# Performance work log

Measured on AMD Instinct MI355X. Metric: run time of the kernel, lower is better.

## Reference

```python
import jax, jax.numpy as jnp
import numpy as np

N, E, D, ED, H = 50000, 800000, 128, 16, 1
EPS = 1e-5


def setup_inputs() -> dict:
    key = jax.random.key(0)
    ks = jax.random.split(key, 12)
    return {
        "x": jax.random.normal(ks[0], (N, D), jnp.float32),
        "edge_index": jax.random.randint(ks[1], (2, E), 0, N),
        "edge_attr": jax.random.normal(ks[2], (E, ED), jnp.float32),
        # GATv2Conv params
        "W_l": jax.random.normal(ks[3], (D, H * D), jnp.float32) / np.sqrt(D),
        "b_l": jnp.zeros((H * D,), jnp.float32),
        "W_r": jax.random.normal(ks[4], (D, H * D), jnp.float32) / np.sqrt(D),
        "b_r": jnp.zeros((H * D,), jnp.float32),
        "W_e": jax.random.normal(ks[5], (ED, H * D), jnp.float32) / np.sqrt(ED),
        "att": jax.random.normal(ks[6], (H, D), jnp.float32) * 0.1,
        "bias_gat": jnp.zeros((D,), jnp.float32),
        # block params
        "weight1": jax.random.normal(ks[7], (2,), jnp.float32),
        "bn1_gamma": jnp.ones((D,), jnp.float32),
        "bn1_beta": jnp.zeros((D,), jnp.float32),
        "conv_w": jax.random.normal(ks[8], (D, D, 3), jnp.float32) / np.sqrt(3 * D),
        "conv_b": jnp.zeros((D,), jnp.float32),
        "weight2": jax.random.normal(ks[9], (2,), jnp.float32),
        "bn2_gamma": jnp.ones((D,), jnp.float32),
        "bn2_beta": jnp.zeros((D,), jnp.float32),
    }


def _batch_norm(z, gamma, beta):
    # NodeLevelBatchNorm in training mode: stats over all nodes of the batch graph
    mu = z.mean(axis=0)
    var = z.var(axis=0)
    return (z - mu) * jax.lax.rsqrt(var + EPS) * gamma + beta


def _gatv2(x, edge_index, edge_attr, W_l, b_l, W_r, b_r, W_e, att, bias_gat):
    n = x.shape[0]
    # add self loops with edge_attr fill_value=0
    loop = jnp.arange(n)
    src = jnp.concatenate([edge_index[0], loop])  # message sources j
    dst = jnp.concatenate([edge_index[1], loop])  # message targets i
    x_l = (x @ W_l + b_l).reshape(n, H, D)
    x_r = (x @ W_r + b_r).reshape(n, H, D)
    e = (edge_attr @ W_e).reshape(-1, H, D)
    e = jnp.concatenate([e, jnp.zeros((n, H, D), e.dtype)], axis=0)  # zeros: lin_edge(0)=0
    # [E+N, H, D] edge messages
    m = jax.nn.leaky_relu(x_l[src] + x_r[dst] + e, negative_slope=0.2)
    logits = jnp.einsum('ehc,hc->eh', m, att)  # [E+N, H]
    # softmax grouped by target node (every node has a self loop -> no empty segments)
    lmax = jax.ops.segment_max(logits, dst, num_segments=n)
    p = jnp.exp(logits - lmax[dst])
    denom = jax.ops.segment_sum(p, dst, num_segments=n)
    alpha = p / denom[dst]
    out = jax.ops.segment_sum(alpha[:, :, None] * x_l[src], dst, num_segments=n)  # [N,H,D]
    return out.mean(axis=1) + bias_gat  # concat=False -> head mean


def reference(x, edge_index, edge_attr, W_l, b_l, W_r, b_r, W_e, att, bias_gat,
              weight1, bn1_gamma, bn1_beta, conv_w, conv_b, weight2,
              bn2_gamma, bn2_beta):
    attn_feat = _gatv2(x, edge_index, edge_attr, W_l, b_l, W_r, b_r, W_e, att, bias_gat)
    w1 = jax.nn.softmax(weight1)
    z = w1[0] * x + w1[1] * attn_feat
    z = _batch_norm(z, bn1_gamma, bn1_beta)
    # Conv1d over the node dimension: [1, C, N] -> [1, C, N]
    z1 = jax.lax.conv_general_dilated(
        z.T[None], conv_w, window_strides=(1,), padding=[(1, 1)],
        dimension_numbers=('NCH', 'OIH', 'NCH'))
    z1 = z1[0].T + conv_b  # [N, C]
    z1 = jax.nn.leaky_relu(z1, negative_slope=0.01)  # dropout inactive in eval
    w2 = jax.nn.softmax(weight2)
    z = w2[0] * z + w2[1] * z1
    z = _batch_norm(z, bn2_gamma, bn2_beta)
    return z
```

## Files before the change

kernel.cpp:

```cpp
#include <hip/hip_runtime.h>
#include <hip/hip_bf16.h>
#include <math.h>

#define DD 128
#define EPSBN 1e-5f

typedef float f2 __attribute__((ext_vector_type(2)));

__device__ __forceinline__ float4 f4_add(float4 a, float4 b) {
    return make_float4(a.x + b.x, a.y + b.y, a.z + b.z, a.w + b.w);
}
__device__ __forceinline__ float4 f4_fma(float a, float4 b, float4 c) {
    c.x = fmaf(a, b.x, c.x); c.y = fmaf(a, b.y, c.y);
    c.z = fmaf(a, b.z, c.z); c.w = fmaf(a, b.w, c.w);
    return c;
}
__device__ __forceinline__ float leakyf(float v, float s) { return v > 0.f ? v : s * v; }

__device__ __forceinline__ unsigned short f2bf(float f) {
    unsigned u = __float_as_uint(f);
    return (unsigned short)((u + 0x7fffu + ((u >> 16) & 1u)) >> 16);
}
__device__ __forceinline__ f2 bfu2f2(unsigned u) {
    f2 r;
    r.x = __uint_as_float(u << 16);
    r.y = __uint_as_float(u & 0xFFFF0000u);
    return r;
}
__device__ __forceinline__ f2 leaky2(f2 v, float s) {
    f2 z = (f2)0.f;
    return __builtin_elementwise_max(v, z) + s * __builtin_elementwise_min(v, z);
}

__global__ __launch_bounds__(256) void k_prep(const float* __restrict__ conv_w, float* __restrict__ wT,
                                              int* __restrict__ counts, float* __restrict__ stats,
                                              int n, int nstats) {
    int idx = blockIdx.x * 256 + threadIdx.x;
    if (idx < 3 * 128 * 128) {
        int k = idx >> 14;
        int r = idx & 16383;
        int ci = r >> 7, co = r & 127;
        wT[idx] = conv_w[(size_t)co * 384 + ci * 3 + k];
    }
    int z = idx - 3 * 128 * 128;
    if (z >= 0) {
        if (z < n) counts[z] = 0;
        else if (z - n < nstats) stats[z - n] = 0.f;
    }
}

__global__ __launch_bounds__(256) void k_gemm_xlxr(
    const float* __restrict__ x, const float* __restrict__ Wl, const float* __restrict__ bl,
    const float* __restrict__ Wr, const float* __restrict__ br,
    float* __restrict__ XR, unsigned short* __restrict__ XLh, int n)
{
    __shared__ float As[64 * 33];
    __shared__ float Bs[32 * 256];
    int tid = threadIdx.x;
    int r0 = blockIdx.x * 64;
    int tx = tid & 31, ty = tid >> 5;

    float4 accL[8], accR[8];
    #pragma unroll
    for (int j = 0; j < 8; ++j) {
        accL[j] = make_float4(0.f, 0.f, 0.f, 0.f);
        accR[j] = make_float4(0.f, 0.f, 0.f, 0.f);
    }

    for (int k0 = 0; k0 < 128; k0 += 32) {
        for (int idx = tid; idx < 64 * 32; idx += 256) {
            int lrow = idx >> 5, kk = idx & 31;
            int g = r0 + lrow;
            As[lrow * 33 + kk] = (g < n) ? x[(size_t)g * DD + k0 + kk] : 0.f;
        }
        for (int idx = tid; idx < 2048; idx += 256) {
            int kk = idx >> 6, co4 = idx & 63;
            float4 v;
            if (co4 < 32) v = ((const float4*)Wl)[(size_t)(k0 + kk) * 32 + co4];
            else          v = ((const float4*)Wr)[(size_t)(k0 + kk) * 32 + (co4 - 32)];
            ((float4*)Bs)[kk * 64 + co4] = v;
        }
        __syncthreads();

        #pragma unroll 4
        for (int kk = 0; kk < 32; ++kk) {
            float a[8];
            #pragma unroll
            for (int j = 0; j < 8; ++j) a[j] = As[(ty * 8 + j) * 33 + kk];
            float4 bL = ((float4*)Bs)[kk * 64 + tx];
            float4 bR = ((float4*)Bs)[kk * 64 + 32 + tx];
            #pragma unroll
            for (int j = 0; j < 8; ++j) {
                accL[j] = f4_fma(a[j], bL, accL[j]);
                accR[j] = f4_fma(a[j], bR, accR[j]);
            }
        }
        __syncthreads();
    }

    float4 blv = ((const float4*)bl)[tx];
    float4 brv = ((const float4*)br)[tx];
    #pragma unroll
    for (int j = 0; j < 8; ++j) {
        int row = r0 + ty * 8 + j;
        if (row < n) {
            float4 L4 = f4_add(accL[j], blv);
            ((float4*)(XR + (size_t)row * DD))[tx] = f4_add(accR[j], brv);
            uint2 hp;
            hp.x = (unsigned)f2bf(L4.x) | ((unsigned)f2bf(L4.y) << 16);
            hp.y = (unsigned)f2bf(L4.z) | ((unsigned)f2bf(L4.w) << 16);
            ((uint2*)(XLh + (size_t)row * DD))[tx] = hp;
        }
    }
}

__global__ __launch_bounds__(256) void k_hist(const int* __restrict__ dst, int* __restrict__ counts, int e) {
    int idx = blockIdx.x * 256 + threadIdx.x;
    if (idx < e) atomicAdd(&counts[dst[idx]], 1);
}

__global__ __launch_bounds__(256) void k_scan1(const int* __restrict__ counts,
                                               int* __restrict__ offsets, int* __restrict__ bsum, int n) {
    __shared__ int tmp[256];
    int t = threadIdx.x;
    int i = blockIdx.x * 256 + t;
    int v = (i < n) ? counts[i] : 0;
    tmp[t] = v;
    __syncthreads();
    for (int off = 1; off < 256; off <<= 1) {
        int u = (t >= off) ? tmp[t - off] : 0;
        __syncthreads();
        tmp[t] += u;
        __syncthreads();
    }
    if (i < n) offsets[i] = tmp[t] - v;
    if (t == 255) bsum[blockIdx.x] = tmp[255];
}

__global__ __launch_bounds__(1024) void k_scan2(int* __restrict__ bsum, int nchunks) {
    __shared__ int tmp[1024];
    int t = threadIdx.x;
    int v = (t < nchunks) ? bsum[t] : 0;
    tmp[t] = v;
    __syncthreads();
    for (int off = 1; off < 1024; off <<= 1) {
        int u = (t >= off) ? tmp[t - off] : 0;
        __syncthreads();
        tmp[t] += u;
        __syncthreads();
    }
    if (t < nchunks) bsum[t] = tmp[t] - v;
    if (t == 0) bsum[nchunks] = tmp[nchunks - 1];
}

__global__ __launch_bounds__(256) void k_scan3(int* __restrict__ offsets, int* __restrict__ cursor,
                                               const int* __restrict__ bsum, int n, int nchunks) {
    int i = blockIdx.x * 256 + threadIdx.x;
    if (i < n) {
        int o = offsets[i] + bsum[i >> 8];
        offsets[i] = o;
        cursor[i] = o;
    }
    if (i == n) offsets[n] = bsum[nchunks];
}

__global__ __launch_bounds__(256) void k_scatter(const int* __restrict__ src, const int* __restrict__ dst,
                                                 int* __restrict__ cursor, int2* __restrict__ epair, int e) {
    int idx = blockIdx.x * 256 + threadIdx.x;
    if (idx >= e) return;
    int d = dst[idx];
    int pos = atomicAdd(&cursor[d], 1);
    epair[pos] = make_int2(idx, src[idx]);
}

#define GAT_LOAD(q_, U0_, U1_, A0_, A1_)                                        \
    {                                                                           \
        int2 g0_ = epair[q_], g1_ = epair[(q_) + 1];                            \
        int e0_ = __builtin_amdgcn_readfirstlane(g0_.x);                        \
        int s0_ = __builtin_amdgcn_readfirstlane(g0_.y);                        \
        int e1_ = __builtin_amdgcn_readfirstlane(g1_.x);                        \
        int s1_ = __builtin_amdgcn_readfirstlane(g1_.y);                        \
        U0_ = XLu[(size_t)s0_ * 64 + lane];                                     \
        U1_ = XLu[(size_t)s1_ * 64 + lane];                                     \
        const float* q0_ = edge_attr + (size_t)e0_ * 16;                        \
        const float* q1_ = edge_attr + (size_t)e1_ * 16;                        \
        _Pragma("unroll")                                                       \
        for (int k_ = 0; k_ < 16; ++k_) { A0_[k_] = q0_[k_]; A1_[k_] = q1_[k_]; } \
    }

#define GAT_COMPUTE(U0_, U1_, A0_, A1_)                                         \
    {                                                                           \
        f2 x0_ = bfu2f2(U0_), x1_ = bfu2f2(U1_);                                \
        f2 ev0_ = (f2)0.f, ev1_ = (f2)0.f;                                      \
        _Pragma("unroll")                                                       \
        for (int k_ = 0; k_ < 16; ++k_) {                                       \
            ev0_ = __builtin_elementwise_fma((f2)A0_[k_], w2[k_], ev0_);        \
            ev1_ = __builtin_elementwise_fma((f2)A1_[k_], w2[k_], ev1_);        \
        }                                                                       \
        f2 m0_ = leaky2(x0_ + xr2 + ev0_, 0.2f);                                \
        f2 m1_ = leaky2(x1_ + xr2 + ev1_, 0.2f);                                \
        float l0_ = m0_.x * att2.x + m0_.y * att2.y;                            \
        float l1_ = m1_.x * att2.x + m1_.y * att2.y;                            \
        _Pragma("unroll")                                                       \
        for (int off_ = 32; off_ > 0; off_ >>= 1) {                             \
            l0_ += __shfl_xor(l0_, off_, 64);                                   \
            l1_ += __shfl_xor(l1_, off_, 64);                                   \
        }                                                                       \
        float g0_ = __expf(l0_), g1_ = __expf(l1_);                             \
        S += g0_ + g1_;                                                         \
        axy = __builtin_elementwise_fma((f2)g0_, x0_, axy);                     \
        axy = __builtin_elementwise_fma((f2)g1_, x1_, axy);                     \
    }

__global__ __launch_bounds__(256) void k_gat(
    const unsigned short* __restrict__ XLh, const float* __restrict__ XR,
    const float* __restrict__ x,
    const int2* __restrict__ epair, const int* __restrict__ offsets,
    const float* __restrict__ edge_attr, const float* __restrict__ We,
    const float* __restrict__ att, const float* __restrict__ bias_gat,
    const float* __restrict__ weight1, float* __restrict__ Z, int n, int nwaves)
{
    int wid  = blockIdx.x * 4 + (threadIdx.x >> 6);
    int lane = threadIdx.x & 63;
    int c = lane * 2;
    const unsigned* __restrict__ XLu = (const unsigned*)XLh;

    f2 w2[16];
    #pragma unroll
    for (int k = 0; k < 16; ++k) w2[k] = *(const f2*)(We + k * DD + c);
    f2 att2 = *(const f2*)(att + c);
    f2 bg   = *(const f2*)(bias_gat + c);
    float w0 = weight1[0], w1v = weight1[1];
    float mw = fmaxf(w0, w1v);
    float e0w = __expf(w0 - mw), e1w = __expf(w1v - mw);
    float winv = 1.f / (e0w + e1w);
    float w1x = e0w * winv, w1a = e1w * winv;

    for (int i = wid; i < n; i += nwaves) {
        f2 xr2 = *(const f2*)(XR + (size_t)i * DD + c);
        f2 xli = bfu2f2(XLu[(size_t)i * 64 + lane]);

        f2 ms = leaky2(xli + xr2, 0.2f);
        float sl = ms.x * att2.x + ms.y * att2.y;
        #pragma unroll
        for (int off = 32; off > 0; off >>= 1) sl += __shfl_xor(sl, off, 64);
        float gs = __expf(sl);
        float S = gs;
        f2 axy = gs * xli;

        int p  = __builtin_amdgcn_readfirstlane(offsets[i]);
        int pe = __builtin_amdgcn_readfirstlane(offsets[i + 1]);
        int cnt = pe - p;
        int np = cnt >> 1;

        unsigned uA0, uA1, uB0, uB1;
        float aA0[16], aA1[16], aB0[16], aB1[16];

        if (np > 0) {
            GAT_LOAD(p, uA0, uA1, aA0, aA1);
            int t = 0;
            for (;;) {
                if (t + 1 < np) GAT_LOAD(p + 2 * (t + 1), uB0, uB1, aB0, aB1);
                GAT_COMPUTE(uA0, uA1, aA0, aA1);
                if (++t >= np) break;
                if (t + 1 < np) GAT_LOAD(p + 2 * (t + 1), uA0, uA1, aA0, aA1);
                GAT_COMPUTE(uB0, uB1, aB0, aB1);
                if (++t >= np) break;
            }
        }
        if (cnt & 1) {
            int2 ej = epair[pe - 1];
            int eid = __builtin_amdgcn_readfirstlane(ej.x);
            int srn = __builtin_amdgcn_readfirstlane(ej.y);
            unsigned u = XLu[(size_t)srn * 64 + lane];
            const float* pa = edge_attr + (size_t)eid * 16;
            f2 ev = (f2)0.f;
            #pragma unroll
            for (int k = 0; k < 16; ++k) ev = __builtin_elementwise_fma((f2)pa[k], w2[k], ev);
            f2 x0 = bfu2f2(u);
            f2 m = leaky2(x0 + xr2 + ev, 0.2f);
            float l = m.x * att2.x + m.y * att2.y;
            #pragma unroll
            for (int off = 32; off > 0; off >>= 1) l += __shfl_xor(l, off, 64);
            float g = __expf(l);
            S += g;
            axy = __builtin_elementwise_fma((f2)g, x0, axy);
        }

        float rl = 1.f / S;
        f2 av = axy * rl + bg;
        f2 xv = *(const f2*)(x + (size_t)i * DD + c);
        f2 zv = w1x * xv + w1a * av;
        *(f2*)(Z + (size_t)i * DD + c) = zv;
    }
}

__global__ __launch_bounds__(256) void k_bn_stats(const float* __restrict__ Zin,
                                                  float* __restrict__ sums, float* __restrict__ sumsq, int n) {
    __shared__ float4 Ls[8][32];
    __shared__ float4 Lq[8][32];
    int tid = threadIdx.x;
    int cg = tid & 31, ry = tid >> 5;
    float4 s = make_float4(0.f, 0.f, 0.f, 0.f), q = s;
    for (int r = blockIdx.x * 8 + ry; r < n; r += gridDim.x * 8) {
        float4 v = ((const float4*)(Zin + (size_t)r * DD))[cg];
        s = f4_add(s, v);
        q.x = fmaf(v.x, v.x, q.x); q.y = fmaf(v.y, v.y, q.y);
        q.z = fmaf(v.z, v.z, q.z); q.w = fmaf(v.w, v.w, q.w);
    }
    Ls[ry][cg] = s; Lq[ry][cg] = q;
    __syncthreads();
    if (tid < 32) {
        float4 ts = Ls[0][tid], tq = Lq[0][tid];
        #pragma unroll
        for (int j = 1; j < 8; ++j) { ts = f4_add(ts, Ls[j][tid]); tq = f4_add(tq, Lq[j][tid]); }
        atomicAdd(&sums[tid * 4 + 0], ts.x); atomicAdd(&sums[tid * 4 + 1], ts.y);
        atomicAdd(&sums[tid * 4 + 2], ts.z); atomicAdd(&sums[tid * 4 + 3], ts.w);
        atomicAdd(&sumsq[tid * 4 + 0], tq.x); atomicAdd(&sumsq[tid * 4 + 1], tq.y);
        atomicAdd(&sumsq[tid * 4 + 2], tq.z); atomicAdd(&sumsq[tid * 4 + 3], tq.w);
    }
}

__global__ __launch_bounds__(128) void k_bn_finish(const float* __restrict__ sums, const float* __restrict__ sumsq,
                                                   const float* __restrict__ gamma, const float* __restrict__ beta,
                                                   float* __restrict__ scale, float* __restrict__ shift, int n) {
    int t = threadIdx.x;
    if (t >= 128) return;
    float fn = (float)n;
    float mu = sums[t] / fn;
    float var = sumsq[t] / fn - mu * mu;
    float rstd = rsqrtf(var + EPSBN);
    float sc = gamma[t] * rstd;
    scale[t] = sc;
    shift[t] = fmaf(-mu, sc, beta[t]);
}

__global__ __launch_bounds__(256) void k_conv(
    const float* __restrict__ Z, const float* __restrict__ scale1, const float* __restrict__ shift1,
    const float* __restrict__ wT, const float* __restrict__ conv_b,
    const float* __restrict__ weight2, float* __restrict__ Z2, int n)
{
    __shared__ float As[66 * 33];
    __shared__ float Bs[3 * 32 * 128];
    int tid = threadIdx.x;
    int r0 = blockIdx.x * 64;
    int tx = tid & 31, ty = tid >> 5;
    int rbase = ty * 8;

    float4 acc[8];
    #pragma unroll
    for (int j = 0; j < 8; ++j) acc[j] = make_float4(0.f, 0.f, 0.f, 0.f);

    for (int ci0 = 0; ci0 < 128; ci0 += 32) {
        for (int idx = tid; idx < 66 * 32; idx += 256) {
            int lrow = idx >> 5, ci = idx & 31;
            int g = r0 - 1 + lrow;
            int cc = ci0 + ci;
            float v = 0.f;
            if (g >= 0 && g < n)
                v = fmaf(Z[(size_t)g * DD + cc], scale1[cc], shift1[cc]);
            As[lrow * 33 + ci] = v;
        }
        for (int idx = tid; idx < 3072; idx += 256) {
            int k = idx >> 10;
            int r = idx & 1023;
            int ci = r >> 5, co4 = r & 31;
            ((float4*)Bs)[idx] = ((const float4*)wT)[(size_t)k * 4096 + (ci0 + ci) * 32 + co4];
        }
        __syncthreads();

        #pragma unroll 2
        for (int ci = 0; ci < 32; ++ci) {
            float a[10];
            #pragma unroll
            for (int j = 0; j < 10; ++j) a[j] = As[(rbase + j) * 33 + ci];
            float4 b0 = ((float4*)Bs)[(0 * 32 + ci) * 32 + tx];
            float4 b1 = ((float4*)Bs)[(1 * 32 + ci) * 32 + tx];
            float4 b2 = ((float4*)Bs)[(2 * 32 + ci) * 32 + tx];
            #pragma unroll
            for (int j = 0; j < 8; ++j) {
                acc[j] = f4_fma(a[j],     b0, acc[j]);
                acc[j] = f4_fma(a[j + 1], b1, acc[j]);
                acc[j] = f4_fma(a[j + 2], b2, acc[j]);
            }
        }
        __syncthreads();
    }

    float w0 = weight2[0], w1v = weight2[1];
    float mw = fmaxf(w0, w1v);
    float e0 = __expf(w0 - mw), e1 = __expf(w1v - mw);
    float winv = 1.f / (e0 + e1);
    float w2x = e0 * winv, w2a = e1 * winv;

    float4 cb = ((const float4*)conv_b)[tx];
    float4 sc1 = ((const float4*)scale1)[tx];
    float4 sh1 = ((const float4*)shift1)[tx];
    #pragma unroll
    for (int j = 0; j < 8; ++j) {
        int row = r0 + rbase + j;
        if (row >= n) break;
        float4 z1 = f4_add(acc[j], cb);
        z1.x = leakyf(z1.x, 0.01f); z1.y = leakyf(z1.y, 0.01f);
        z1.z = leakyf(z1.z, 0.01f); z1.w = leakyf(z1.w, 0.01f);
        float4 zv = ((const float4*)(Z + (size_t)row * DD))[tx];
        float4 zbn;
        zbn.x = fmaf(zv.x, sc1.x, sh1.x); zbn.y = fmaf(zv.y, sc1.y, sh1.y);
        zbn.z = fmaf(zv.z, sc1.z, sh1.z); zbn.w = fmaf(zv.w, sc1.w, sh1.w);
        float4 o;
        o.x = w2x * zbn.x + w2a * z1.x; o.y = w2x * zbn.y + w2a * z1.y;
        o.z = w2x * zbn.z + w2a * z1.z; o.w = w2x * zbn.w + w2a * z1.w;
        ((float4*)(Z2 + (size_t)row * DD))[tx] = o;
    }
}

__global__ __launch_bounds__(256) void k_final(const float* __restrict__ Z2,
                                               const float* __restrict__ scale2, const float* __restrict__ shift2,
                                               float* __restrict__ out, int total4) {
    int idx = blockIdx.x * 256 + threadIdx.x;
    if (idx >= total4) return;
    int c4 = idx & 31;
    float4 v = ((const float4*)Z2)[idx];
    float4 sc = ((const float4*)scale2)[c4];
    float4 sh = ((const float4*)shift2)[c4];
    float4 r;
    r.x = fmaf(v.x, sc.x, sh.x); r.y = fmaf(v.y, sc.y, sh.y);
    r.z = fmaf(v.z, sc.z, sh.z); r.w = fmaf(v.w, sc.w, sh.w);
    ((float4*)out)[idx] = r;
}

extern "C" void kernel_launch(void* const* d_in, const int* in_sizes, int n_in,
                              void* d_out, int out_size, void* d_ws, size_t ws_size,
                              hipStream_t stream)
{
    const float* x          = (const float*)d_in[0];
    const int*   edge_index = (const int*)d_in[1];
    const float* edge_attr  = (const float*)d_in[2];
    const float* W_l        = (const float*)d_in[3];
    const float* b_l        = (const float*)d_in[4];
    const float* W_r        = (const float*)d_in[5];
    const float* b_r        = (const float*)d_in[6];
    const float* W_e        = (const float*)d_in[7];
    const float* att        = (const float*)d_in[8];
    const float* bias_gat   = (const float*)d_in[9];
    const float* weight1    = (const float*)d_in[10];
    const float* bn1_gamma  = (const float*)d_in[11];
    const float* bn1_beta   = (const float*)d_in[12];
    const float* conv_w     = (const float*)d_in[13];
    const float* conv_b     = (const float*)d_in[14];
    const float* weight2    = (const float*)d_in[15];
    const float* bn2_gamma  = (const float*)d_in[16];
    const float* bn2_beta   = (const float*)d_in[17];

    int n = in_sizes[0] / DD;
    int e = in_sizes[1] / 2;
    int nchunks = (n + 255) / 256;

    float* XR = (float*)d_ws;
    float* Z  = XR + (size_t)n * DD;
    float* wT = Z + (size_t)n * DD;
    float* stats = wT + 49152;
    float* sums1 = stats,       *sumsq1 = stats + 128;
    float* sums2 = stats + 256, *sumsq2 = stats + 384;
    float* scale1 = stats + 512, *shift1 = stats + 640;
    float* scale2 = stats + 768, *shift2 = stats + 896;
    int* counts  = (int*)(stats + 1024);
    int* offsets = counts + n;
    int* cursor  = offsets + n + 2;
    int* bsum    = cursor + n;
    int2* epair  = (int2*)(bsum + ((nchunks + 2) & ~1));
    unsigned short* XLh = (unsigned short*)(epair + e);
    float* Z2 = XR;

    const int* src = edge_index;
    const int* dst = edge_index + e;

    const int nwaves = 8192;

    k_prep<<<(3 * 128 * 128 + n + 512 + 255) / 256, 256, 0, stream>>>(conv_w, wT, counts, stats, n, 512);
    k_gemm_xlxr<<<(n + 63) / 64, 256, 0, stream>>>(x, W_l, b_l, W_r, b_r, XR, XLh, n);
    k_hist<<<(e + 255) / 256, 256, 0, stream>>>(dst, counts, e);
    k_scan1<<<nchunks, 256, 0, stream>>>(counts, offsets, bsum, n);
    k_scan2<<<1, 1024, 0, stream>>>(bsum, nchunks);
    k_scan3<<<(n + 256) / 256, 256, 0, stream>>>(offsets, cursor, bsum, n, nchunks);
    k_scatter<<<(e + 255) / 256, 256, 0, stream>>>(src, dst, cursor, epair, e);
    k_gat<<<nwaves / 4, 256, 0, stream>>>(XLh, XR, x, epair, offsets,
                                          edge_attr, W_e, att, bias_gat, weight1, Z, n, nwaves);
    k_bn_stats<<<256, 256, 0, stream>>>(Z, sums1, sumsq1, n);
    k_bn_finish<<<1, 128, 0, stream>>>(sums1, sumsq1, bn1_gamma, bn1_beta, scale1, shift1, n);
    k_conv<<<(n + 63) / 64, 256, 0, stream>>>(Z, scale1, shift1, wT, conv_b, weight2, Z2, n);
    k_bn_stats<<<256, 256, 0, stream>>>(Z2, sums2, sumsq2, n);
    k_bn_finish<<<1, 128, 0, stream>>>(sums2, sumsq2, bn2_gamma, bn2_beta, scale2, shift2, n);
    k_final<<<(n * 32 + 255) / 256, 256, 0, stream>>>(Z2, scale2, shift2, (float*)d_out, n * 32);
}
```

Before: 612.9 us.

## Batch GAT edges in fours with cooperative edge_attr loads; fuse BN2 stats into conv

The GAT aggregation loop now handles four edges per step instead of two. Each lane loads one edge_attr element, and the values are staged through a per-wave double-buffered LDS slot, replacing sixteen redundant per-lane scalar loads per edge. Separately, the conv kernel accumulates per-channel sum and sum-of-squares of its output and adds them to the global stats with atomics, which removes the separate k_bn_stats pass that re-read Z2. The costs are extra LDS traffic and a tail loop for up to three leftover edges. The global float atomics also make the summation order nondeterministic.

```diff
diff --git a/kernel.cpp b/kernel.cpp
--- a/kernel.cpp
+++ b/kernel.cpp
@@ -173,44 +173,71 @@
     epair[pos] = make_int2(idx, src[idx]);
 }
 
-#define GAT_LOAD(q_, U0_, U1_, A0_, A1_)                                        \
-    {                                                                           \
-        int2 g0_ = epair[q_], g1_ = epair[(q_) + 1];                            \
-        int e0_ = __builtin_amdgcn_readfirstlane(g0_.x);                        \
-        int s0_ = __builtin_amdgcn_readfirstlane(g0_.y);                        \
-        int e1_ = __builtin_amdgcn_readfirstlane(g1_.x);                        \
-        int s1_ = __builtin_amdgcn_readfirstlane(g1_.y);                        \
-        U0_ = XLu[(size_t)s0_ * 64 + lane];                                     \
-        U1_ = XLu[(size_t)s1_ * 64 + lane];                                     \
-        const float* q0_ = edge_attr + (size_t)e0_ * 16;                        \
-        const float* q1_ = edge_attr + (size_t)e1_ * 16;                        \
-        _Pragma("unroll")                                                       \
-        for (int k_ = 0; k_ < 16; ++k_) { A0_[k_] = q0_[k_]; A1_[k_] = q1_[k_]; } \
-    }
-
-#define GAT_COMPUTE(U0_, U1_, A0_, A1_)                                         \
-    {                                                                           \
-        f2 x0_ = bfu2f2(U0_), x1_ = bfu2f2(U1_);                                \
-        f2 ev0_ = (f2)0.f, ev1_ = (f2)0.f;                                      \
-        _Pragma("unroll")                                                       \
-        for (int k_ = 0; k_ < 16; ++k_) {                                       \
-            ev0_ = __builtin_elementwise_fma((f2)A0_[k_], w2[k_], ev0_);        \
-            ev1_ = __builtin_elementwise_fma((f2)A1_[k_], w2[k_], ev1_);        \
-        }                                                                       \
-        f2 m0_ = leaky2(x0_ + xr2 + ev0_, 0.2f);                                \
-        f2 m1_ = leaky2(x1_ + xr2 + ev1_, 0.2f);                                \
-        float l0_ = m0_.x * att2.x + m0_.y * att2.y;                            \
-        float l1_ = m1_.x * att2.x + m1_.y * att2.y;                            \
-        _Pragma("unroll")                                                       \
-        for (int off_ = 32; off_ > 0; off_ >>= 1) {                             \
-            l0_ += __shfl_xor(l0_, off_, 64);                                   \
-            l1_ += __shfl_xor(l1_, off_, 64);                                   \
-        }                                                                       \
-        float g0_ = __expf(l0_), g1_ = __expf(l1_);                             \
-        S += g0_ + g1_;                                                         \
-        axy = __builtin_elementwise_fma((f2)g0_, x0_, axy);                     \
-        axy = __builtin_elementwise_fma((f2)g1_, x1_, axy);                     \
-    }
+
+#define EPROJ(EB_, J_, EV_) {                                                   \
+    const float4* e4_ = ((const float4*)(EB_)) + (J_) * 4;                      \
+    float4 a0_ = e4_[0], a1_ = e4_[1], a2_ = e4_[2], a3_ = e4_[3];              \
+    f2 v_ = (f2)0.f;                                                            \
+    v_ = __builtin_elementwise_fma((f2)a0_.x, w2[0],  v_);                      \
+    v_ = __builtin_elementwise_fma((f2)a0_.y, w2[1],  v_);                      \
+    v_ = __builtin_elementwise_fma((f2)a0_.z, w2[2],  v_);                      \
+    v_ = __builtin_elementwise_fma((f2)a0_.w, w2[3],  v_);                      \
+    v_ = __builtin_elementwise_fma((f2)a1_.x, w2[4],  v_);                      \
+    v_ = __builtin_elementwise_fma((f2)a1_.y, w2[5],  v_);                      \
+    v_ = __builtin_elementwise_fma((f2)a1_.z, w2[6],  v_);                      \
+    v_ = __builtin_elementwise_fma((f2)a1_.w, w2[7],  v_);                      \
+    v_ = __builtin_elementwise_fma((f2)a2_.x, w2[8],  v_);                      \
+    v_ = __builtin_elementwise_fma((f2)a2_.y, w2[9],  v_);                      \
+    v_ = __builtin_elementwise_fma((f2)a2_.z, w2[10], v_);                      \
+    v_ = __builtin_elementwise_fma((f2)a2_.w, w2[11], v_);                      \
+    v_ = __builtin_elementwise_fma((f2)a3_.x, w2[12], v_);                      \
+    v_ = __builtin_elementwise_fma((f2)a3_.y, w2[13], v_);                      \
+    v_ = __builtin_elementwise_fma((f2)a3_.z, w2[14], v_);                      \
+    v_ = __builtin_elementwise_fma((f2)a3_.w, w2[15], v_);                      \
+    EV_ = v_; }
+
+#define GAT_LOAD4(q_, U0_, U1_, U2_, U3_, AV_) {                                \
+    int2 g0_ = epair[q_], g1_ = epair[(q_) + 1];                                \
+    int2 g2_ = epair[(q_) + 2], g3_ = epair[(q_) + 3];                          \
+    int s0_ = __builtin_amdgcn_readfirstlane(g0_.y);                            \
+    int s1_ = __builtin_amdgcn_readfirstlane(g1_.y);                            \
+    int s2_ = __builtin_amdgcn_readfirstlane(g2_.y);                            \
+    int s3_ = __builtin_amdgcn_readfirstlane(g3_.y);                            \
+    U0_ = XLu[(size_t)s0_ * 64 + lane];                                         \
+    U1_ = XLu[(size_t)s1_ * 64 + lane];                                         \
+    U2_ = XLu[(size_t)s2_ * 64 + lane];                                         \
+    U3_ = XLu[(size_t)s3_ * 64 + lane];                                         \
+    int ej_ = esel == 0 ? g0_.x : esel == 1 ? g1_.x : esel == 2 ? g2_.x : g3_.x;\
+    AV_ = edge_attr[(size_t)ej_ * 16 + ek]; }
+
+#define GAT_COMPUTE4(U0_, U1_, U2_, U3_, EB_) {                                 \
+    f2 x0_ = bfu2f2(U0_), x1_ = bfu2f2(U1_);                                    \
+    f2 x2_ = bfu2f2(U2_), x3_ = bfu2f2(U3_);                                    \
+    f2 ev0_, ev1_, ev2_, ev3_;                                                  \
+    EPROJ(EB_, 0, ev0_); EPROJ(EB_, 1, ev1_);                                   \
+    EPROJ(EB_, 2, ev2_); EPROJ(EB_, 3, ev3_);                                   \
+    f2 m0_ = leaky2(x0_ + xr2 + ev0_, 0.2f);                                    \
+    f2 m1_ = leaky2(x1_ + xr2 + ev1_, 0.2f);                                    \
+    f2 m2_ = leaky2(x2_ + xr2 + ev2_, 0.2f);                                    \
+    f2 m3_ = leaky2(x3_ + xr2 + ev3_, 0.2f);                                    \
+    float l0_ = m0_.x * att2.x + m0_.y * att2.y;                                \
+    float l1_ = m1_.x * att2.x + m1_.y * att2.y;                                \
+    float l2_ = m2_.x * att2.x + m2_.y * att2.y;                                \
+    float l3_ = m3_.x * att2.x + m3_.y * att2.y;                                \
+    _Pragma("unroll")                                                           \
+    for (int off_ = 32; off_ > 0; off_ >>= 1) {                                 \
+        l0_ += __shfl_xor(l0_, off_, 64);                                       \
+        l1_ += __shfl_xor(l1_, off_, 64);                                       \
+        l2_ += __shfl_xor(l2_, off_, 64);                                       \
+        l3_ += __shfl_xor(l3_, off_, 64);                                       \
+    }                                                                           \
+    float g0_ = __expf(l0_), g1_ = __expf(l1_);                                 \
+    float g2_ = __expf(l2_), g3_ = __expf(l3_);                                 \
+    S += (g0_ + g1_) + (g2_ + g3_);                                             \
+    axy = __builtin_elementwise_fma((f2)g0_, x0_, axy);                         \
+    axy = __builtin_elementwise_fma((f2)g1_, x1_, axy);                         \
+    axy = __builtin_elementwise_fma((f2)g2_, x2_, axy);                         \
+    axy = __builtin_elementwise_fma((f2)g3_, x3_, axy); }
 
 __global__ __launch_bounds__(256) void k_gat(
     const unsigned short* __restrict__ XLh, const float* __restrict__ XR,
@@ -220,10 +247,15 @@
     const float* __restrict__ att, const float* __restrict__ bias_gat,
     const float* __restrict__ weight1, float* __restrict__ Z, int n, int nwaves)
 {
-    int wid  = blockIdx.x * 4 + (threadIdx.x >> 6);
+    __shared__ float ebuf[4][2][64];
+    int wv   = threadIdx.x >> 6;
+    int wid  = blockIdx.x * 4 + wv;
     int lane = threadIdx.x & 63;
     int c = lane * 2;
+    int esel = lane >> 4, ek = lane & 15;
     const unsigned* __restrict__ XLu = (const unsigned*)XLh;
+    float* ebA = &ebuf[wv][0][0];
+    float* ebB = &ebuf[wv][1][0];
 
     f2 w2[16];
     #pragma unroll
@@ -251,25 +283,29 @@
         int p  = __builtin_amdgcn_readfirstlane(offsets[i]);
         int pe = __builtin_amdgcn_readfirstlane(offsets[i + 1]);
         int cnt = pe - p;
-        int np = cnt >> 1;
-
-        unsigned uA0, uA1, uB0, uB1;
-        float aA0[16], aA1[16], aB0[16], aB1[16];
-
-        if (np > 0) {
-            GAT_LOAD(p, uA0, uA1, aA0, aA1);
+        int ng = cnt >> 2;
+
+        if (ng > 0) {
+            unsigned uA0, uA1, uA2, uA3, uB0, uB1, uB2, uB3;
+            float avA, avB;
+            GAT_LOAD4(p, uA0, uA1, uA2, uA3, avA);
+            ebA[lane] = avA;
             int t = 0;
             for (;;) {
-                if (t + 1 < np) GAT_LOAD(p + 2 * (t + 1), uB0, uB1, aB0, aB1);
-                GAT_COMPUTE(uA0, uA1, aA0, aA1);
-                if (++t >= np) break;
-                if (t + 1 < np) GAT_LOAD(p + 2 * (t + 1), uA0, uA1, aA0, aA1);
-                GAT_COMPUTE(uB0, uB1, aB0, aB1);
-                if (++t >= np) break;
+                bool mA = (t + 1 < ng);
+                if (mA) GAT_LOAD4(p + 4 * (t + 1), uB0, uB1, uB2, uB3, avB);
+                GAT_COMPUTE4(uA0, uA1, uA2, uA3, ebA);
+                if (mA) ebB[lane] = avB;
+                if (++t >= ng) break;
+                bool mB = (t + 1 < ng);
+                if (mB) GAT_LOAD4(p + 4 * (t + 1), uA0, uA1, uA2, uA3, avA);
+                GAT_COMPUTE4(uB0, uB1, uB2, uB3, ebB);
+                if (mB) ebA[lane] = avA;
+                if (++t >= ng) break;
             }
         }
-        if (cnt & 1) {
-            int2 ej = epair[pe - 1];
+        for (int q = p + (ng << 2); q < pe; ++q) {
+            int2 ej = epair[q];
             int eid = __builtin_amdgcn_readfirstlane(ej.x);
             int srn = __builtin_amdgcn_readfirstlane(ej.y);
             unsigned u = XLu[(size_t)srn * 64 + lane];
@@ -338,7 +374,8 @@
 __global__ __launch_bounds__(256) void k_conv(
     const float* __restrict__ Z, const float* __restrict__ scale1, const float* __restrict__ shift1,
     const float* __restrict__ wT, const float* __restrict__ conv_b,
-    const float* __restrict__ weight2, float* __restrict__ Z2, int n)
+    const float* __restrict__ weight2, float* __restrict__ Z2,
+    float* __restrict__ sums2, float* __restrict__ sumsq2, int n)
 {
     __shared__ float As[66 * 33];
     __shared__ float Bs[3 * 32 * 128];
@@ -396,6 +433,7 @@
     float4 cb = ((const float4*)conv_b)[tx];
     float4 sc1 = ((const float4*)scale1)[tx];
     float4 sh1 = ((const float4*)shift1)[tx];
+    float4 s4 = make_float4(0.f, 0.f, 0.f, 0.f), q4 = s4;
     #pragma unroll
     for (int j = 0; j < 8; ++j) {
         int row = r0 + rbase + j;
@@ -411,6 +449,24 @@
         o.x = w2x * zbn.x + w2a * z1.x; o.y = w2x * zbn.y + w2a * z1.y;
         o.z = w2x * zbn.z + w2a * z1.z; o.w = w2x * zbn.w + w2a * z1.w;
         ((float4*)(Z2 + (size_t)row * DD))[tx] = o;
+        s4 = f4_add(s4, o);
+        q4.x = fmaf(o.x, o.x, q4.x); q4.y = fmaf(o.y, o.y, q4.y);
+        q4.z = fmaf(o.z, o.z, q4.z); q4.w = fmaf(o.w, o.w, q4.w);
+    }
+
+    float4* rs = (float4*)As;
+    float4* rq = rs + 256;
+    rs[ty * 32 + tx] = s4;
+    rq[ty * 32 + tx] = q4;
+    __syncthreads();
+    if (tid < 32) {
+        float4 ts = rs[tid], tq = rq[tid];
+        #pragma unroll
+        for (int j = 1; j < 8; ++j) { ts = f4_add(ts, rs[j * 32 + tid]); tq = f4_add(tq, rq[j * 32 + tid]); }
+        atomicAdd(&sums2[tid * 4 + 0], ts.x); atomicAdd(&sums2[tid * 4 + 1], ts.y);
+        atomicAdd(&sums2[tid * 4 + 2], ts.z); atomicAdd(&sums2[tid * 4 + 3], ts.w);
+        atomicAdd(&sumsq2[tid * 4 + 0], tq.x); atomicAdd(&sumsq2[tid * 4 + 1], tq.y);
+        atomicAdd(&sumsq2[tid * 4 + 2], tq.z); atomicAdd(&sumsq2[tid * 4 + 3], tq.w);
     }
 }
 
@@ -488,8 +544,8 @@
                                           edge_attr, W_e, att, bias_gat, weight1, Z, n, nwaves);
     k_bn_stats<<<256, 256, 0, stream>>>(Z, sums1, sumsq1, n);
     k_bn_finish<<<1, 128, 0, stream>>>(sums1, sumsq1, bn1_gamma, bn1_beta, scale1, shift1, n);
-    k_conv<<<(n + 63) / 64, 256, 0, stream>>>(Z, scale1, shift1, wT, conv_b, weight2, Z2, n);
-    k_bn_stats<<<256, 256, 0, stream>>>(Z2, sums2, sumsq2, n);
+    k_conv<<<(n + 63) / 64, 256, 0, stream>>>(Z, scale1, shift1, wT, conv_b, weight2, Z2,
+                                              sums2, sumsq2, n);
     k_bn_finish<<<1, 128, 0, stream>>>(sums2, sumsq2, bn2_gamma, bn2_beta, scale2, shift2, n);
     k_final<<<(n * 32 + 255) / 256, 256, 0, stream>>>(Z2, scale2, shift2, (float*)d_out, n * 32);
 }
```

Measured after the change: 598.5 us. -2.4%, faster.
